# Kernel tuning notes

Measured on AMD Instinct MI355X. Metric: run time of the kernel, lower is better.

## Reference

```python
import jax, jax.numpy as jnp
import numpy as np

USER, ITEM, TAG = 100000, 50000, 20000
D = 64
LAYERS = 2
LEAKY = 0.5
KEEP = 0.9
E_ADJ, E_TAG, E_SOC = 2_000_000, 1_000_000, 1_000_000


def _xavier(k, shape):
    bound = float(np.sqrt(6.0 / (shape[0] + shape[1])))
    return jax.random.uniform(k, shape, jnp.float32, -bound, bound)


def setup_inputs() -> dict:
    key = jax.random.key(0)
    ks = jax.random.split(key, 12)
    N = USER + ITEM   # interaction graph nodes
    M = ITEM + TAG    # tag graph nodes
    return {
        "uEmbeds": _xavier(ks[0], (USER, D)),
        "iEmbeds": _xavier(ks[1], (ITEM, D)),
        "tEmbeds": _xavier(ks[2], (TAG, D)),
        "adj_rows": jax.random.randint(ks[3], (E_ADJ,), 0, N, jnp.int32),
        "adj_cols": jax.random.randint(ks[4], (E_ADJ,), 0, N, jnp.int32),
        "adj_vals": jax.random.uniform(ks[5], (E_ADJ,), jnp.float32) * 0.01,
        "tag_rows": jax.random.randint(ks[6], (E_TAG,), 0, M, jnp.int32),
        "tag_cols": jax.random.randint(ks[7], (E_TAG,), 0, M, jnp.int32),
        "tag_vals": jax.random.uniform(ks[8], (E_TAG,), jnp.float32) * 0.01,
        "soc_rows": jax.random.randint(ks[9], (E_SOC,), 0, USER, jnp.int32),
        "soc_cols": jax.random.randint(ks[10], (E_SOC,), 0, USER, jnp.int32),
        "soc_vals": jax.random.uniform(ks[11], (E_SOC,), jnp.float32) * 0.01,
    }


def _drop_edge(vals, k):
    # SpAdjDropEdge: keep each edge w.p. KEEP, rescale kept values by 1/KEEP.
    # Masking values to 0 is equivalent to removing edges from the spmm.
    mask = jnp.floor(jax.random.uniform(k, vals.shape) + KEEP)
    return vals * mask * (1.0 / KEEP)


def _gcn(rows, cols, vals, x, n):
    # spmm: out[r] = sum_e vals[e] * x[cols[e]]  (gather-scale-scatter)
    h = jax.ops.segment_sum(vals[:, None] * x[cols], rows, num_segments=n)
    return jnp.where(h >= 0, h, LEAKY * h)  # LeakyReLU


def reference(uEmbeds, iEmbeds, tEmbeds,
              adj_rows, adj_cols, adj_vals,
              tag_rows, tag_cols, tag_vals,
              soc_rows, soc_cols, soc_vals):
    dkey = jax.random.key(42)
    lat = jnp.concatenate([uEmbeds, iEmbeds], axis=0)       # [USER+ITEM, D]
    tag_lat = jnp.concatenate([iEmbeds, tEmbeds], axis=0)   # [ITEM+TAG, D]
    acc = lat
    for i in range(LAYERS):
        k1 = jax.random.fold_in(dkey, 3 * i)
        k2 = jax.random.fold_in(dkey, 3 * i + 1)
        k3 = jax.random.fold_in(dkey, 3 * i + 2)
        tem = _gcn(adj_rows, adj_cols, _drop_edge(adj_vals, k1), lat, USER + ITEM)
        tg_in = jnp.concatenate([lat[USER:], tag_lat[ITEM:]], axis=0)
        tg = _gcn(tag_rows, tag_cols, _drop_edge(tag_vals, k2), tg_in, ITEM + TAG)
        soc = _gcn(soc_rows, soc_cols, _drop_edge(soc_vals, k3), lat[:USER], USER)
        lat = jnp.concatenate([tem[:USER] + soc, tem[USER:] + tg[:ITEM]], axis=0)
        tag_lat = tg
        acc = acc + lat
    return acc  # embeds = sum(lats), shape [USER+ITEM, D]
```

## Files before the change

### kernel.cpp

```cpp
#include <hip/hip_runtime.h>
#include <stdint.h>

#define USER_N 100000
#define ITEM_N 50000
#define TAG_N  20000
#define NN (USER_N + ITEM_N)
#define MM (ITEM_N + TAG_N)
#define DD 64
#define NT_ROWS (NN + MM + USER_N)

#define BSH 10
#define BROWS (1 << BSH)
#define NBKT0 147
#define NBKT1 167
#define NBKT (NBKT0 + NBKT1)
#define SLICES 512

__host__ __device__ __forceinline__ void tf2x32(uint32_t k0, uint32_t k1,
                                                uint32_t x0, uint32_t x1,
                                                uint32_t* o0, uint32_t* o1) {
  uint32_t ks2 = k0 ^ k1 ^ 0x1BD11BDAu;
#define ROTL32(v, d) (((v) << (d)) | ((v) >> (32 - (d))))
#define TF_RND(d) { x0 += x1; x1 = ROTL32(x1, d); x1 ^= x0; }
  x0 += k0; x1 += k1;
  TF_RND(13) TF_RND(15) TF_RND(26) TF_RND(6)
  x0 += k1;  x1 += ks2 + 1u;
  TF_RND(17) TF_RND(29) TF_RND(16) TF_RND(24)
  x0 += ks2; x1 += k0 + 2u;
  TF_RND(13) TF_RND(15) TF_RND(26) TF_RND(6)
  x0 += k0;  x1 += k1 + 3u;
  TF_RND(17) TF_RND(29) TF_RND(16) TF_RND(24)
  x0 += k1;  x1 += ks2 + 4u;
  TF_RND(13) TF_RND(15) TF_RND(26) TF_RND(6)
  x0 += ks2; x1 += k0 + 5u;
  *o0 = x0; *o1 = x1;
#undef TF_RND
#undef ROTL32
}

__device__ __forceinline__ float drop_mask(uint32_t e, uint32_t k0, uint32_t k1) {
  uint32_t o0, o1;
  tf2x32(k0, k1, 0u, e, &o0, &o1);
  uint32_t bits = o0 ^ o1;
  float u = __uint_as_float((bits >> 9) | 0x3F800000u) - 1.0f;
  return floorf(u + 0.9f);
}

__device__ __forceinline__ uint32_t f2bf(float f) {
  uint32_t u = __float_as_uint(f);
  return (u + 0x7fffu + ((u >> 16) & 1u)) >> 16;
}
__device__ __forceinline__ float bflo(uint32_t u) { return __uint_as_float(u << 16); }
__device__ __forceinline__ float bfhi(uint32_t u) { return __uint_as_float(u & 0xffff0000u); }


__global__ __launch_bounds__(1024) void hist_kernel(
    const int* __restrict__ adj_r, const int* __restrict__ tag_r,
    const int* __restrict__ soc_r, int* __restrict__ chist,
    int nAdj, int nTag, int nSoc) {
  __shared__ int cnt[NBKT1];
  int tid = threadIdx.x, k = blockIdx.x;
  int r = (k >= SLICES) ? 1 : 0;
  int kk = k - r * SLICES;
  int nTot = r ? (nTag + nSoc) : nAdj;
  int nBkt = r ? NBKT1 : NBKT0;
  int bktBase = r ? NBKT0 : 0;
  for (int b = tid; b < nBkt; b += 1024) cnt[b] = 0;
  __syncthreads();
  int per = (nTot + SLICES - 1) / SLICES;
  int e0 = kk * per;
  int e1 = e0 + per; if (e1 > nTot) e1 = nTot;
  for (int e = e0 + tid; e < e1; e += 1024) {
    int j;
    if (r == 0) j = adj_r[e];
    else if (e < nTag) j = tag_r[e];
    else j = MM + soc_r[e - nTag];
    atomicAdd(&cnt[j >> BSH], 1);
  }
  __syncthreads();
  for (int b = tid; b < nBkt; b += 1024)
    chist[(bktBase + b) * SLICES + kk] = cnt[b];
}

__global__ __launch_bounds__(512) void scanA_kernel(const int* __restrict__ chist,
                                                    int* __restrict__ btot) {
  __shared__ int red[512];
  int gb = blockIdx.x, t = threadIdx.x;
  red[t] = chist[gb * SLICES + t];
  __syncthreads();
  for (int off = 256; off > 0; off >>= 1) {
    if (t < off) red[t] += red[t + off];
    __syncthreads();
  }
  if (t == 0) btot[gb] = red[0];
}

__global__ __launch_bounds__(512) void scanB_kernel(const int* __restrict__ chist,
                                                    const int* __restrict__ btot,
                                                    int* __restrict__ boff,
                                                    int* __restrict__ bbase,
                                                    int* __restrict__ rp, int totE) {
  __shared__ int red[512];
  int gb = blockIdx.x, t = threadIdx.x;
  int rstart = (gb >= NBKT0) ? NBKT0 : 0;
  int ps = 0;
  for (int b = rstart + t; b < gb; b += 512) ps += btot[b];
  red[t] = ps;
  __syncthreads();
  for (int off = 256; off > 0; off >>= 1) {
    if (t < off) red[t] += red[t + off];
    __syncthreads();
  }
  int pb = red[0];
  __syncthreads();
  int c = chist[gb * SLICES + t];
  red[t] = c;
  __syncthreads();
  for (int off = 1; off < 512; off <<= 1) {
    int v = (t >= off) ? red[t - off] : 0;
    __syncthreads();
    red[t] += v;
    __syncthreads();
  }
  boff[gb * SLICES + t] = pb + red[t] - c;
  if (t == 0) {
    bbase[gb] = pb;
    if (gb == 0) rp[NT_ROWS] = totE;
  }
}

__global__ __launch_bounds__(1024) void bin_kernel(
    const int* __restrict__ pr, const int* __restrict__ pc, const float* __restrict__ pv,
    const int* __restrict__ sr, const int* __restrict__ scc, const float* __restrict__ sv,
    const int* __restrict__ boff, int2* __restrict__ stage,
    int nPrim, int nTot, int rowOff2, int bktBase, int nBkt,
    uint32_t pa0, uint32_t pa1, uint32_t pb0, uint32_t pb1,
    uint32_t sa0, uint32_t sa1, uint32_t sb0, uint32_t sb1) {
  __shared__ int cur[NBKT1];
  int tid = threadIdx.x, k = blockIdx.x;
  for (int b = tid; b < nBkt; b += 1024) cur[b] = boff[(bktBase + b) * SLICES + k];
  __syncthreads();
  int per = (nTot + SLICES - 1) / SLICES;
  int e0 = k * per;
  int e1 = e0 + per; if (e1 > nTot) e1 = nTot;
  const float SC = (float)(1.0 / 0.9);
  for (int e = e0 + tid; e < e1; e += 1024) {
    int j, c; float v; uint32_t le, k00, k01, k10, k11;
    if (e < nPrim) {
      le = (uint32_t)e;
      j = pr[e]; c = pc[e]; v = pv[e];
      k00 = pa0; k01 = pa1; k10 = pb0; k11 = pb1;
    } else {
      le = (uint32_t)(e - nPrim);
      j = rowOff2 + sr[e - nPrim]; c = scc[e - nPrim]; v = sv[e - nPrim];
      k00 = sa0; k01 = sa1; k10 = sb0; k11 = sb1;
    }
    uint32_t w = f2bf(v * drop_mask(le, k00, k01) * SC) |
                 (f2bf(v * drop_mask(le, k10, k11) * SC) << 16);
    int lb = j >> BSH;
    int pos = atomicAdd(&cur[lb], 1);
    stage[pos] = make_int2(c | ((j & (BROWS - 1)) << 18), (int)w);
  }
}

__global__ __launch_bounds__(512) void ls_kernel(
    int* __restrict__ rp, const int* __restrict__ bbase, const int* __restrict__ btot,
    const int2* __restrict__ stage, int2* __restrict__ rec,
    int rowStart, int rowEnd, int eBase, int bktBase) {
  __shared__ int cur[BROWS];
  __shared__ int red[512];
  int tid = threadIdx.x, lb = blockIdx.x, gb = bktBase + lb;
  int sbase = bbase[gb];
  int nst = btot[gb];
  int base = eBase + sbase;
  cur[tid] = 0; cur[tid + 512] = 0;
  __syncthreads();
  for (int i = tid; i < nst; i += 512)
    atomicAdd(&cur[((uint32_t)stage[sbase + i].x) >> 18], 1);
  __syncthreads();
  int c0 = cur[2 * tid], c1 = cur[2 * tid + 1];
  int pairs = c0 + c1;
  red[tid] = pairs;
  __syncthreads();
  for (int off = 1; off < 512; off <<= 1) {
    int v = (tid >= off) ? red[tid - off] : 0;
    __syncthreads();
    red[tid] += v;
    __syncthreads();
  }
  int excl = red[tid] - pairs;
  int r = rowStart + (lb << BSH) + 2 * tid;
  int p0 = base + excl, p1 = p0 + c0;
  if (r < rowEnd) rp[r] = p0;
  if (r + 1 < rowEnd) rp[r + 1] = p1;
  __syncthreads();
  cur[2 * tid] = p0; cur[2 * tid + 1] = p1;
  __syncthreads();
  for (int i = tid; i < nst; i += 512) {
    int2 m = stage[sbase + i];
    int pos = atomicAdd(&cur[((uint32_t)m.x) >> 18], 1);
    rec[pos] = make_int2((m.x & 0x3FFFF) * DD, m.y);
  }
}

#define FMA8(c0, c1, v, q) { \
    c0.x += v * bflo(q.x); c0.y += v * bfhi(q.x); \
    c0.z += v * bflo(q.y); c0.w += v * bfhi(q.y); \
    c1.x += v * bflo(q.z); c1.y += v * bfhi(q.z); \
    c1.z += v * bflo(q.w); c1.w += v * bfhi(q.w); }

template <int VS>
__device__ __forceinline__ void gather_sub(int s0, int s1, const int2* __restrict__ rec,
                                           const ushort* __restrict__ src,
                                           int fl, float4& A0, float4& A1) {
  float4 a0 = make_float4(0.f, 0.f, 0.f, 0.f);
  float4 a1 = make_float4(0.f, 0.f, 0.f, 0.f);
  float4 b0 = make_float4(0.f, 0.f, 0.f, 0.f);
  float4 b1 = make_float4(0.f, 0.f, 0.f, 0.f);
  const ushort* sl = src + fl * 8;
  int i = s0;
  for (; i + 8 <= s1; i += 8) {
    long long r[8];
    uint4 q[8];
#pragma unroll
    for (int u = 0; u < 8; ++u)
      r[u] = __builtin_nontemporal_load((const long long*)(rec + i + u));
#pragma unroll
    for (int u = 0; u < 8; ++u)
      q[u] = *(const uint4*)(sl + (uint32_t)r[u]);
#pragma unroll
    for (int u = 0; u < 8; ++u) {
      uint32_t w = (uint32_t)((unsigned long long)r[u] >> 32);
      float v = VS ? bfhi(w) : bflo(w);
      if (u & 1) { FMA8(b0, b1, v, q[u]) } else { FMA8(a0, a1, v, q[u]) }
    }
  }
  if (i + 4 <= s1) {
    long long r[4];
    uint4 q[4];
#pragma unroll
    for (int u = 0; u < 4; ++u)
      r[u] = __builtin_nontemporal_load((const long long*)(rec + i + u));
#pragma unroll
    for (int u = 0; u < 4; ++u)
      q[u] = *(const uint4*)(sl + (uint32_t)r[u]);
#pragma unroll
    for (int u = 0; u < 4; ++u) {
      uint32_t w = (uint32_t)((unsigned long long)r[u] >> 32);
      float v = VS ? bfhi(w) : bflo(w);
      if (u & 1) { FMA8(b0, b1, v, q[u]) } else { FMA8(a0, a1, v, q[u]) }
    }
    i += 4;
  }
  for (; i < s1; ++i) {
    long long rr = __builtin_nontemporal_load((const long long*)(rec + i));
    uint4 q = *(const uint4*)(sl + (uint32_t)rr);
    uint32_t w = (uint32_t)((unsigned long long)rr >> 32);
    float v = VS ? bfhi(w) : bflo(w);
    FMA8(a0, a1, v, q)
  }
  A0 = make_float4(a0.x + b0.x, a0.y + b0.y, a0.z + b0.z, a0.w + b0.w);
  A1 = make_float4(a1.x + b1.x, a1.y + b1.y, a1.z + b1.z, a1.w + b1.w);
}

__device__ __forceinline__ float4 lk4(float4 x) {
  x.x = x.x >= 0.0f ? x.x : 0.5f * x.x;
  x.y = x.y >= 0.0f ? x.y : 0.5f * x.y;
  x.z = x.z >= 0.0f ? x.z : 0.5f * x.z;
  x.w = x.w >= 0.0f ? x.w : 0.5f * x.w;
  return x;
}

__device__ __forceinline__ uint4 pack8(float4 a, float4 b) {
  uint4 p;
  p.x = f2bf(a.x) | (f2bf(a.y) << 16);
  p.y = f2bf(a.z) | (f2bf(a.w) << 16);
  p.z = f2bf(b.x) | (f2bf(b.y) << 16);
  p.w = f2bf(b.z) | (f2bf(b.w) << 16);
  return p;
}

template <int VS, bool FINAL, bool WITHTAG>
__global__ void gather_mega_kernel(
    const int* __restrict__ arp, const int2* __restrict__ arec,
    const int* __restrict__ srp, const int2* __restrict__ srec,
    const int* __restrict__ trp, const int2* __restrict__ trec,
    const ushort* __restrict__ lat,
    ushort* __restrict__ latOut, ushort* __restrict__ tgOut,
    float* __restrict__ acc) {
  int r = (blockIdx.x * blockDim.x + threadIdx.x) >> 3;
  int fl = threadIdx.x & 7;
  if (WITHTAG && r >= NN) {
    int rr = r - NN;
    if (rr >= TAG_N) return;
    int tr = rr + ITEM_N;
    float4 a0, a1;
    gather_sub<VS>(trp[tr], trp[tr + 1], trec, lat + (size_t)USER_N * DD, fl, a0, a1);
    ((uint4*)(tgOut + (size_t)rr * DD))[fl] = pack8(lk4(a0), lk4(a1));
    return;
  }
  if (r >= NN) return;
  float4 t0, t1, b0, b1;
  gather_sub<VS>(arp[r], arp[r + 1], arec, lat, fl, t0, t1);
  if (r < USER_N) {
    gather_sub<VS>(srp[r], srp[r + 1], srec, lat, fl, b0, b1);
  } else {
    int tr = r - USER_N;
    gather_sub<VS>(trp[tr], trp[tr + 1], trec, lat + (size_t)USER_N * DD, fl, b0, b1);
  }
  t0 = lk4(t0); t1 = lk4(t1); b0 = lk4(b0); b1 = lk4(b1);
  float4 o0 = make_float4(t0.x + b0.x, t0.y + b0.y, t0.z + b0.z, t0.w + b0.w);
  float4 o1 = make_float4(t1.x + b1.x, t1.y + b1.y, t1.z + b1.z, t1.w + b1.w);
  if (FINAL) {
    uint4 l = ((const uint4*)(lat + (size_t)r * DD))[fl];
    float4* ap = (float4*)(acc + (size_t)r * DD);
    float4 v0 = ap[fl * 2], v1 = ap[fl * 2 + 1];
    v0.x += bflo(l.x) + o0.x; v0.y += bfhi(l.x) + o0.y;
    v0.z += bflo(l.y) + o0.z; v0.w += bfhi(l.y) + o0.w;
    v1.x += bflo(l.z) + o1.x; v1.y += bfhi(l.z) + o1.y;
    v1.z += bflo(l.w) + o1.z; v1.w += bfhi(l.w) + o1.w;
    ap[fl * 2] = v0; ap[fl * 2 + 1] = v1;
  } else {
    ((uint4*)(latOut + (size_t)r * DD))[fl] = pack8(o0, o1);
  }
}

__global__ void init_kernel(const float4* __restrict__ u, const float4* __restrict__ it,
                            const float4* __restrict__ tE,
                            float4* __restrict__ acc, ushort4* __restrict__ lat0bf,
                            ushort4* __restrict__ tEmbf) {
  int idx = blockIdx.x * blockDim.x + threadIdx.x;
  const int uN = USER_N * 16, nN = NN * 16;
  if (idx < nN) {
    float4 v = (idx < uN) ? u[idx] : it[idx - uN];
    acc[idx] = v;
    ushort4 h;
    h.x = (ushort)f2bf(v.x); h.y = (ushort)f2bf(v.y);
    h.z = (ushort)f2bf(v.z); h.w = (ushort)f2bf(v.w);
    lat0bf[idx] = h;
  } else if (idx < nN + TAG_N * 16) {
    int j = idx - nN;
    float4 v = tE[j];
    ushort4 h;
    h.x = (ushort)f2bf(v.x); h.y = (ushort)f2bf(v.y);
    h.z = (ushort)f2bf(v.z); h.w = (ushort)f2bf(v.w);
    tEmbf[j] = h;
  }
}

extern "C" void kernel_launch(void* const* d_in, const int* in_sizes, int n_in,
                              void* d_out, int out_size, void* d_ws, size_t ws_size,
                              hipStream_t stream) {
  const float* uE    = (const float*)d_in[0];
  const float* iE    = (const float*)d_in[1];
  const float* tEm   = (const float*)d_in[2];
  const int*   adj_r = (const int*)d_in[3];
  const int*   adj_c = (const int*)d_in[4];
  const float* adj_v = (const float*)d_in[5];
  const int*   tag_r = (const int*)d_in[6];
  const int*   tag_c = (const int*)d_in[7];
  const float* tag_v = (const float*)d_in[8];
  const int*   soc_r = (const int*)d_in[9];
  const int*   soc_c = (const int*)d_in[10];
  const float* soc_v = (const float*)d_in[11];
  const int nAdj = in_sizes[5], nTag = in_sizes[8], nSoc = in_sizes[11];
  const int totE = nAdj + nTag + nSoc;

  float* acc = (float*)d_out;

  ushort* lat0bf = (ushort*)d_ws;
  ushort* tEmbf  = lat0bf + (size_t)NN * DD;
  ushort* lat1bf = tEmbf  + (size_t)TAG_N * DD;
  ushort* tg1bf  = lat1bf + (size_t)NN * DD;
  int2* stage    = (int2*)lat1bf;
  int2* rec  = (int2*)(tg1bf + (size_t)TAG_N * DD);
  int*  ip   = (int*)(rec + totE);
  int* chist = ip;  ip += NBKT * SLICES;
  int* boff  = ip;  ip += NBKT * SLICES;
  int* btot  = ip;  ip += NBKT;
  int* bbase = ip;  ip += NBKT;
  int* rp    = ip;  ip += NT_ROWS + 1;

  uint32_t kk[6][2];
  for (uint32_t j = 0; j < 6; ++j) tf2x32(0u, 42u, 0u, j, &kk[j][0], &kk[j][1]);

  const int thr = 256;
#define CDIV(a, b) (((a) + (b) - 1) / (b))

  hist_kernel<<<2 * SLICES, 1024, 0, stream>>>(adj_r, tag_r, soc_r, chist,
                                               nAdj, nTag, nSoc);
  scanA_kernel<<<NBKT, 512, 0, stream>>>(chist, btot);
  scanB_kernel<<<NBKT, 512, 0, stream>>>(chist, btot, boff, bbase, rp, totE);
  bin_kernel<<<SLICES, 1024, 0, stream>>>(
      adj_r, adj_c, adj_v, adj_r, adj_c, adj_v,
      boff, stage, nAdj, nAdj, 0, 0, NBKT0,
      kk[0][0], kk[0][1], kk[3][0], kk[3][1], 0u, 0u, 0u, 0u);
  ls_kernel<<<NBKT0, 512, 0, stream>>>(rp, bbase, btot, stage, rec, 0, NN, 0, 0);
  bin_kernel<<<SLICES, 1024, 0, stream>>>(
      tag_r, tag_c, tag_v, soc_r, soc_c, soc_v,
      boff, stage, nTag, nTag + nSoc, MM, NBKT0, NBKT1,
      kk[1][0], kk[1][1], kk[4][0], kk[4][1],
      kk[2][0], kk[2][1], kk[5][0], kk[5][1]);
  ls_kernel<<<NBKT1, 512, 0, stream>>>(rp, bbase, btot, stage, rec, NN, NT_ROWS, nAdj, NBKT0);

  init_kernel<<<CDIV((NN + TAG_N) * 16, thr), thr, 0, stream>>>(
      (const float4*)uE, (const float4*)iE, (const float4*)tEm,
      (float4*)acc, (ushort4*)lat0bf, (ushort4*)tEmbf);

  const int* arp = rp;
  const int* trp = rp + NN;
  const int* srp = rp + NN + MM;
  gather_mega_kernel<0, false, true><<<CDIV((NN + TAG_N) * 8, thr), thr, 0, stream>>>(
      arp, rec, srp, rec, trp, rec, lat0bf, lat1bf, tg1bf, nullptr);

  gather_mega_kernel<1, true, false><<<CDIV(NN * 8, thr), thr, 0, stream>>>(
      arp, rec, srp, rec, trp, rec, lat1bf, nullptr, nullptr, acc);
#undef CDIV
}
```

Before: 419.2 us.

## Sort edges within rows by column chunk and fuse init into histogram kernel

The local-sort kernel now counts and scatters edges into (row, column-chunk) sub-buckets, so each row's edges come out ordered by coarse column range. The aim is better cache locality for the later gathers of source embeddings. Separately, the embedding init and bf16 conversion work moves into extra blocks of the histogram kernel, removing one launch. The cost is a 10x larger shared-memory counter array and more atomics and scan work in the local sort.

```diff
diff --git a/kernel.cpp b/kernel.cpp
--- a/kernel.cpp
+++ b/kernel.cpp
@@ -15,6 +15,8 @@
 #define NBKT1 167
 #define NBKT (NBKT0 + NBKT1)
 #define SLICES 512
+#define NCH 10
+#define CSH2 14
 
 __host__ __device__ __forceinline__ void tf2x32(uint32_t k0, uint32_t k1,
                                                 uint32_t x0, uint32_t x1,
@@ -54,12 +56,35 @@
 __device__ __forceinline__ float bfhi(uint32_t u) { return __uint_as_float(u & 0xffff0000u); }
 
 
-__global__ __launch_bounds__(1024) void hist_kernel(
+__global__ __launch_bounds__(1024) void histinit_kernel(
     const int* __restrict__ adj_r, const int* __restrict__ tag_r,
     const int* __restrict__ soc_r, int* __restrict__ chist,
-    int nAdj, int nTag, int nSoc) {
+    int nAdj, int nTag, int nSoc,
+    const float4* __restrict__ u, const float4* __restrict__ it,
+    const float4* __restrict__ tE, float4* __restrict__ acc,
+    ushort4* __restrict__ lat0bf, ushort4* __restrict__ tEmbf) {
   __shared__ int cnt[NBKT1];
   int tid = threadIdx.x, k = blockIdx.x;
+  if (k >= 2 * SLICES) {
+    int idx = (k - 2 * SLICES) * 1024 + tid;
+    const int uN = USER_N * 16, nN = NN * 16;
+    if (idx < nN) {
+      float4 v = (idx < uN) ? u[idx] : it[idx - uN];
+      acc[idx] = v;
+      ushort4 h;
+      h.x = (ushort)f2bf(v.x); h.y = (ushort)f2bf(v.y);
+      h.z = (ushort)f2bf(v.z); h.w = (ushort)f2bf(v.w);
+      lat0bf[idx] = h;
+    } else if (idx < nN + TAG_N * 16) {
+      int j = idx - nN;
+      float4 v = tE[j];
+      ushort4 h;
+      h.x = (ushort)f2bf(v.x); h.y = (ushort)f2bf(v.y);
+      h.z = (ushort)f2bf(v.z); h.w = (ushort)f2bf(v.w);
+      tEmbf[j] = h;
+    }
+    return;
+  }
   int r = (k >= SLICES) ? 1 : 0;
   int kk = k - r * SLICES;
   int nTot = r ? (nTag + nSoc) : nAdj;
@@ -167,20 +192,26 @@
     int* __restrict__ rp, const int* __restrict__ bbase, const int* __restrict__ btot,
     const int2* __restrict__ stage, int2* __restrict__ rec,
     int rowStart, int rowEnd, int eBase, int bktBase) {
-  __shared__ int cur[BROWS];
+  __shared__ int cur[BROWS * NCH];
   __shared__ int red[512];
   int tid = threadIdx.x, lb = blockIdx.x, gb = bktBase + lb;
   int sbase = bbase[gb];
   int nst = btot[gb];
   int base = eBase + sbase;
-  cur[tid] = 0; cur[tid + 512] = 0;
-  __syncthreads();
-  for (int i = tid; i < nst; i += 512)
-    atomicAdd(&cur[((uint32_t)stage[sbase + i].x) >> 18], 1);
-  __syncthreads();
-  int c0 = cur[2 * tid], c1 = cur[2 * tid + 1];
-  int pairs = c0 + c1;
-  red[tid] = pairs;
+  for (int i = tid; i < BROWS * NCH; i += 512) cur[i] = 0;
+  __syncthreads();
+  for (int i = tid; i < nst; i += 512) {
+    int mx = stage[sbase + i].x;
+    atomicAdd(&cur[(((uint32_t)mx) >> 18) * NCH + ((mx & 0x3FFFF) >> CSH2)], 1);
+  }
+  __syncthreads();
+  const int PT = (BROWS * NCH) / 512;
+  int loc[PT];
+  int s = 0;
+  int o0 = tid * PT;
+#pragma unroll
+  for (int u = 0; u < PT; ++u) { loc[u] = s; s += cur[o0 + u]; }
+  red[tid] = s;
   __syncthreads();
   for (int off = 1; off < 512; off <<= 1) {
     int v = (tid >= off) ? red[tid - off] : 0;
@@ -188,18 +219,23 @@
     red[tid] += v;
     __syncthreads();
   }
-  int excl = red[tid] - pairs;
-  int r = rowStart + (lb << BSH) + 2 * tid;
-  int p0 = base + excl, p1 = p0 + c0;
-  if (r < rowEnd) rp[r] = p0;
-  if (r + 1 < rowEnd) rp[r + 1] = p1;
-  __syncthreads();
-  cur[2 * tid] = p0; cur[2 * tid + 1] = p1;
+  int excl = red[tid] - s;
+#pragma unroll
+  for (int u = 0; u < PT; ++u) {
+    int idx = o0 + u;
+    int p = base + excl + loc[u];
+    cur[idx] = p;
+    if ((idx % NCH) == 0) {
+      int r = rowStart + (lb << BSH) + idx / NCH;
+      if (r < rowEnd) rp[r] = p;
+    }
+  }
   __syncthreads();
   for (int i = tid; i < nst; i += 512) {
     int2 m = stage[sbase + i];
-    int pos = atomicAdd(&cur[((uint32_t)m.x) >> 18], 1);
-    rec[pos] = make_int2((m.x & 0x3FFFF) * DD, m.y);
+    int col = m.x & 0x3FFFF;
+    int pos = atomicAdd(&cur[(((uint32_t)m.x) >> 18) * NCH + (col >> CSH2)], 1);
+    rec[pos] = make_int2(col * DD, m.y);
   }
 }
 
@@ -325,29 +361,6 @@
   }
 }
 
-__global__ void init_kernel(const float4* __restrict__ u, const float4* __restrict__ it,
-                            const float4* __restrict__ tE,
-                            float4* __restrict__ acc, ushort4* __restrict__ lat0bf,
-                            ushort4* __restrict__ tEmbf) {
-  int idx = blockIdx.x * blockDim.x + threadIdx.x;
-  const int uN = USER_N * 16, nN = NN * 16;
-  if (idx < nN) {
-    float4 v = (idx < uN) ? u[idx] : it[idx - uN];
-    acc[idx] = v;
-    ushort4 h;
-    h.x = (ushort)f2bf(v.x); h.y = (ushort)f2bf(v.y);
-    h.z = (ushort)f2bf(v.z); h.w = (ushort)f2bf(v.w);
-    lat0bf[idx] = h;
-  } else if (idx < nN + TAG_N * 16) {
-    int j = idx - nN;
-    float4 v = tE[j];
-    ushort4 h;
-    h.x = (ushort)f2bf(v.x); h.y = (ushort)f2bf(v.y);
-    h.z = (ushort)f2bf(v.z); h.w = (ushort)f2bf(v.w);
-    tEmbf[j] = h;
-  }
-}
-
 extern "C" void kernel_launch(void* const* d_in, const int* in_sizes, int n_in,
                               void* d_out, int out_size, void* d_ws, size_t ws_size,
                               hipStream_t stream) {
@@ -387,8 +400,11 @@
   const int thr = 256;
 #define CDIV(a, b) (((a) + (b) - 1) / (b))
 
-  hist_kernel<<<2 * SLICES, 1024, 0, stream>>>(adj_r, tag_r, soc_r, chist,
-                                               nAdj, nTag, nSoc);
+  int initBlocks = CDIV((NN + TAG_N) * 16, 1024);
+  histinit_kernel<<<2 * SLICES + initBlocks, 1024, 0, stream>>>(
+      adj_r, tag_r, soc_r, chist, nAdj, nTag, nSoc,
+      (const float4*)uE, (const float4*)iE, (const float4*)tEm,
+      (float4*)acc, (ushort4*)lat0bf, (ushort4*)tEmbf);
   scanA_kernel<<<NBKT, 512, 0, stream>>>(chist, btot);
   scanB_kernel<<<NBKT, 512, 0, stream>>>(chist, btot, boff, bbase, rp, totE);
   bin_kernel<<<SLICES, 1024, 0, stream>>>(
@@ -403,10 +419,6 @@
       kk[2][0], kk[2][1], kk[5][0], kk[5][1]);
   ls_kernel<<<NBKT1, 512, 0, stream>>>(rp, bbase, btot, stage, rec, NN, NT_ROWS, nAdj, NBKT0);
 
-  init_kernel<<<CDIV((NN + TAG_N) * 16, thr), thr, 0, stream>>>(
-      (const float4*)uE, (const float4*)iE, (const float4*)tEm,
-      (float4*)acc, (ushort4*)lat0bf, (ushort4*)tEmbf);
-
   const int* arp = rp;
   const int* trp = rp + NN;
   const int* srp = rp + NN + MM;
```

Result: no change. 415.5 us (-0.9%).

## Merge hist/init and both bin/ls rounds into single launches; drop acc init

Applied to the files above, without the earlier changes.

Folds the bf16 conversion of the embeddings into the histogram kernel. The two binning passes now run as one launch, using the output buffer as a second staging area, and the two local-sort passes are likewise merged into one launch. The fp32 acc initialisation is removed: the final gather reads the original user/item embeddings directly instead of re-reading acc. The gather inner loop becomes a single 16-wide unrolled masked loop with no 8/4/1 tails, which issues padded loads up to 16 past the end, hence the extra 16 elements reserved after rec. This cuts launches and serialization and removes one full fp32 write and read, at the cost of wasted gather loads on short rows.

```diff
diff --git a/kernel.cpp b/kernel.cpp
--- a/kernel.cpp
+++ b/kernel.cpp
@@ -54,12 +54,34 @@
 __device__ __forceinline__ float bfhi(uint32_t u) { return __uint_as_float(u & 0xffff0000u); }
 
 
-__global__ __launch_bounds__(1024) void hist_kernel(
+__global__ __launch_bounds__(1024) void histinit_kernel(
     const int* __restrict__ adj_r, const int* __restrict__ tag_r,
     const int* __restrict__ soc_r, int* __restrict__ chist,
-    int nAdj, int nTag, int nSoc) {
+    int nAdj, int nTag, int nSoc,
+    const float4* __restrict__ u, const float4* __restrict__ it,
+    const float4* __restrict__ tE,
+    ushort4* __restrict__ lat0bf, ushort4* __restrict__ tEmbf) {
   __shared__ int cnt[NBKT1];
   int tid = threadIdx.x, k = blockIdx.x;
+  if (k >= 2 * SLICES) {
+    int idx = (k - 2 * SLICES) * 1024 + tid;
+    const int uN = USER_N * 16, nN = NN * 16;
+    if (idx < nN) {
+      float4 v = (idx < uN) ? u[idx] : it[idx - uN];
+      ushort4 h;
+      h.x = (ushort)f2bf(v.x); h.y = (ushort)f2bf(v.y);
+      h.z = (ushort)f2bf(v.z); h.w = (ushort)f2bf(v.w);
+      lat0bf[idx] = h;
+    } else if (idx < nN + TAG_N * 16) {
+      int j = idx - nN;
+      float4 v = tE[j];
+      ushort4 h;
+      h.x = (ushort)f2bf(v.x); h.y = (ushort)f2bf(v.y);
+      h.z = (ushort)f2bf(v.z); h.w = (ushort)f2bf(v.w);
+      tEmbf[j] = h;
+    }
+    return;
+  }
   int r = (k >= SLICES) ? 1 : 0;
   int kk = k - r * SLICES;
   int nTot = r ? (nTag + nSoc) : nAdj;
@@ -129,31 +151,43 @@
   }
 }
 
-__global__ __launch_bounds__(1024) void bin_kernel(
-    const int* __restrict__ pr, const int* __restrict__ pc, const float* __restrict__ pv,
-    const int* __restrict__ sr, const int* __restrict__ scc, const float* __restrict__ sv,
-    const int* __restrict__ boff, int2* __restrict__ stage,
-    int nPrim, int nTot, int rowOff2, int bktBase, int nBkt,
-    uint32_t pa0, uint32_t pa1, uint32_t pb0, uint32_t pb1,
-    uint32_t sa0, uint32_t sa1, uint32_t sb0, uint32_t sb1) {
+__global__ __launch_bounds__(1024) void bin01_kernel(
+    const int* __restrict__ adj_r, const int* __restrict__ adj_c, const float* __restrict__ adj_v,
+    const int* __restrict__ tag_r, const int* __restrict__ tag_c, const float* __restrict__ tag_v,
+    const int* __restrict__ soc_r, const int* __restrict__ soc_c, const float* __restrict__ soc_v,
+    const int* __restrict__ boff, int2* __restrict__ stage0, int2* __restrict__ stage1,
+    int nAdj, int nTag, int nSoc,
+    uint32_t a0, uint32_t a1, uint32_t a2, uint32_t a3,
+    uint32_t t0, uint32_t t1, uint32_t t2, uint32_t t3,
+    uint32_t s0, uint32_t s1, uint32_t s2, uint32_t s3) {
   __shared__ int cur[NBKT1];
   int tid = threadIdx.x, k = blockIdx.x;
-  for (int b = tid; b < nBkt; b += 1024) cur[b] = boff[(bktBase + b) * SLICES + k];
+  int rnd = (k >= SLICES) ? 1 : 0;
+  int kk = k - rnd * SLICES;
+  int nTot = rnd ? (nTag + nSoc) : nAdj;
+  int nBkt = rnd ? NBKT1 : NBKT0;
+  int bktBase = rnd ? NBKT0 : 0;
+  int2* stage = rnd ? stage1 : stage0;
+  for (int b = tid; b < nBkt; b += 1024) cur[b] = boff[(bktBase + b) * SLICES + kk];
   __syncthreads();
   int per = (nTot + SLICES - 1) / SLICES;
-  int e0 = k * per;
+  int e0 = kk * per;
   int e1 = e0 + per; if (e1 > nTot) e1 = nTot;
   const float SC = (float)(1.0 / 0.9);
   for (int e = e0 + tid; e < e1; e += 1024) {
     int j, c; float v; uint32_t le, k00, k01, k10, k11;
-    if (e < nPrim) {
+    if (rnd == 0) {
       le = (uint32_t)e;
-      j = pr[e]; c = pc[e]; v = pv[e];
-      k00 = pa0; k01 = pa1; k10 = pb0; k11 = pb1;
+      j = adj_r[e]; c = adj_c[e]; v = adj_v[e];
+      k00 = a0; k01 = a1; k10 = a2; k11 = a3;
+    } else if (e < nTag) {
+      le = (uint32_t)e;
+      j = tag_r[e]; c = tag_c[e]; v = tag_v[e];
+      k00 = t0; k01 = t1; k10 = t2; k11 = t3;
     } else {
-      le = (uint32_t)(e - nPrim);
-      j = rowOff2 + sr[e - nPrim]; c = scc[e - nPrim]; v = sv[e - nPrim];
-      k00 = sa0; k01 = sa1; k10 = sb0; k11 = sb1;
+      le = (uint32_t)(e - nTag);
+      j = MM + soc_r[e - nTag]; c = soc_c[e - nTag]; v = soc_v[e - nTag];
+      k00 = s0; k01 = s1; k10 = s2; k11 = s3;
     }
     uint32_t w = f2bf(v * drop_mask(le, k00, k01) * SC) |
                  (f2bf(v * drop_mask(le, k10, k11) * SC) << 16);
@@ -163,13 +197,19 @@
   }
 }
 
-__global__ __launch_bounds__(512) void ls_kernel(
+__global__ __launch_bounds__(512) void ls01_kernel(
     int* __restrict__ rp, const int* __restrict__ bbase, const int* __restrict__ btot,
-    const int2* __restrict__ stage, int2* __restrict__ rec,
-    int rowStart, int rowEnd, int eBase, int bktBase) {
+    const int2* __restrict__ stage0, const int2* __restrict__ stage1,
+    int2* __restrict__ rec, int nAdj) {
   __shared__ int cur[BROWS];
   __shared__ int red[512];
-  int tid = threadIdx.x, lb = blockIdx.x, gb = bktBase + lb;
+  int tid = threadIdx.x, gb = blockIdx.x;
+  int rnd = (gb >= NBKT0) ? 1 : 0;
+  int lb = rnd ? gb - NBKT0 : gb;
+  const int2* stage = rnd ? stage1 : stage0;
+  int rowStart = rnd ? NN : 0;
+  int rowEnd = rnd ? NT_ROWS : NN;
+  int eBase = rnd ? nAdj : 0;
   int sbase = bbase[gb];
   int nst = btot[gb];
   int base = eBase + sbase;
@@ -218,46 +258,25 @@
   float4 b0 = make_float4(0.f, 0.f, 0.f, 0.f);
   float4 b1 = make_float4(0.f, 0.f, 0.f, 0.f);
   const ushort* sl = src + fl * 8;
-  int i = s0;
-  for (; i + 8 <= s1; i += 8) {
-    long long r[8];
-    uint4 q[8];
+  for (int i = s0; i < s1; i += 16) {
+    int n = s1 - i;
+    long long r[16];
 #pragma unroll
-    for (int u = 0; u < 8; ++u)
+    for (int u = 0; u < 16; ++u)
       r[u] = __builtin_nontemporal_load((const long long*)(rec + i + u));
+    uint4 q[16];
 #pragma unroll
-    for (int u = 0; u < 8; ++u)
-      q[u] = *(const uint4*)(sl + (uint32_t)r[u]);
+    for (int u = 0; u < 16; ++u) {
+      uint32_t off = (u < n) ? (uint32_t)r[u] : 0u;
+      q[u] = *(const uint4*)(sl + off);
+    }
 #pragma unroll
-    for (int u = 0; u < 8; ++u) {
+    for (int u = 0; u < 16; ++u) {
       uint32_t w = (uint32_t)((unsigned long long)r[u] >> 32);
       float v = VS ? bfhi(w) : bflo(w);
+      v = (u < n) ? v : 0.0f;
       if (u & 1) { FMA8(b0, b1, v, q[u]) } else { FMA8(a0, a1, v, q[u]) }
     }
-  }
-  if (i + 4 <= s1) {
-    long long r[4];
-    uint4 q[4];
-#pragma unroll
-    for (int u = 0; u < 4; ++u)
-      r[u] = __builtin_nontemporal_load((const long long*)(rec + i + u));
-#pragma unroll
-    for (int u = 0; u < 4; ++u)
-      q[u] = *(const uint4*)(sl + (uint32_t)r[u]);
-#pragma unroll
-    for (int u = 0; u < 4; ++u) {
-      uint32_t w = (uint32_t)((unsigned long long)r[u] >> 32);
-      float v = VS ? bfhi(w) : bflo(w);
-      if (u & 1) { FMA8(b0, b1, v, q[u]) } else { FMA8(a0, a1, v, q[u]) }
-    }
-    i += 4;
-  }
-  for (; i < s1; ++i) {
-    long long rr = __builtin_nontemporal_load((const long long*)(rec + i));
-    uint4 q = *(const uint4*)(sl + (uint32_t)rr);
-    uint32_t w = (uint32_t)((unsigned long long)rr >> 32);
-    float v = VS ? bfhi(w) : bflo(w);
-    FMA8(a0, a1, v, q)
   }
   A0 = make_float4(a0.x + b0.x, a0.y + b0.y, a0.z + b0.z, a0.w + b0.w);
   A1 = make_float4(a1.x + b1.x, a1.y + b1.y, a1.z + b1.z, a1.w + b1.w);
@@ -286,6 +305,7 @@
     const int* __restrict__ srp, const int2* __restrict__ srec,
     const int* __restrict__ trp, const int2* __restrict__ trec,
     const ushort* __restrict__ lat,
+    const float* __restrict__ uE, const float* __restrict__ iE,
     ushort* __restrict__ latOut, ushort* __restrict__ tgOut,
     float* __restrict__ acc) {
   int r = (blockIdx.x * blockDim.x + threadIdx.x) >> 3;
@@ -313,38 +333,18 @@
   float4 o1 = make_float4(t1.x + b1.x, t1.y + b1.y, t1.z + b1.z, t1.w + b1.w);
   if (FINAL) {
     uint4 l = ((const uint4*)(lat + (size_t)r * DD))[fl];
-    float4* ap = (float4*)(acc + (size_t)r * DD);
-    float4 v0 = ap[fl * 2], v1 = ap[fl * 2 + 1];
+    const float4* e0 = (r < USER_N)
+        ? (const float4*)(uE + (size_t)r * DD)
+        : (const float4*)(iE + (size_t)(r - USER_N) * DD);
+    float4 v0 = e0[fl * 2], v1 = e0[fl * 2 + 1];
     v0.x += bflo(l.x) + o0.x; v0.y += bfhi(l.x) + o0.y;
     v0.z += bflo(l.y) + o0.z; v0.w += bfhi(l.y) + o0.w;
     v1.x += bflo(l.z) + o1.x; v1.y += bfhi(l.z) + o1.y;
     v1.z += bflo(l.w) + o1.z; v1.w += bfhi(l.w) + o1.w;
+    float4* ap = (float4*)(acc + (size_t)r * DD);
     ap[fl * 2] = v0; ap[fl * 2 + 1] = v1;
   } else {
     ((uint4*)(latOut + (size_t)r * DD))[fl] = pack8(o0, o1);
-  }
-}
-
-__global__ void init_kernel(const float4* __restrict__ u, const float4* __restrict__ it,
-                            const float4* __restrict__ tE,
-                            float4* __restrict__ acc, ushort4* __restrict__ lat0bf,
-                            ushort4* __restrict__ tEmbf) {
-  int idx = blockIdx.x * blockDim.x + threadIdx.x;
-  const int uN = USER_N * 16, nN = NN * 16;
-  if (idx < nN) {
-    float4 v = (idx < uN) ? u[idx] : it[idx - uN];
-    acc[idx] = v;
-    ushort4 h;
-    h.x = (ushort)f2bf(v.x); h.y = (ushort)f2bf(v.y);
-    h.z = (ushort)f2bf(v.z); h.w = (ushort)f2bf(v.w);
-    lat0bf[idx] = h;
-  } else if (idx < nN + TAG_N * 16) {
-    int j = idx - nN;
-    float4 v = tE[j];
-    ushort4 h;
-    h.x = (ushort)f2bf(v.x); h.y = (ushort)f2bf(v.y);
-    h.z = (ushort)f2bf(v.z); h.w = (ushort)f2bf(v.w);
-    tEmbf[j] = h;
   }
 }
 
@@ -372,9 +372,10 @@
   ushort* tEmbf  = lat0bf + (size_t)NN * DD;
   ushort* lat1bf = tEmbf  + (size_t)TAG_N * DD;
   ushort* tg1bf  = lat1bf + (size_t)NN * DD;
-  int2* stage    = (int2*)lat1bf;
+  int2* stage0   = (int2*)lat1bf;
+  int2* stage1   = (int2*)d_out;
   int2* rec  = (int2*)(tg1bf + (size_t)TAG_N * DD);
-  int*  ip   = (int*)(rec + totE);
+  int*  ip   = (int*)(rec + totE + 16);
   int* chist = ip;  ip += NBKT * SLICES;
   int* boff  = ip;  ip += NBKT * SLICES;
   int* btot  = ip;  ip += NBKT;
@@ -387,33 +388,28 @@
   const int thr = 256;
 #define CDIV(a, b) (((a) + (b) - 1) / (b))
 
-  hist_kernel<<<2 * SLICES, 1024, 0, stream>>>(adj_r, tag_r, soc_r, chist,
-                                               nAdj, nTag, nSoc);
+  int initBlocks = CDIV((NN + TAG_N) * 16, 1024);
+  histinit_kernel<<<2 * SLICES + initBlocks, 1024, 0, stream>>>(
+      adj_r, tag_r, soc_r, chist, nAdj, nTag, nSoc,
+      (const float4*)uE, (const float4*)iE, (const float4*)tEm,
+      (ushort4*)lat0bf, (ushort4*)tEmbf);
   scanA_kernel<<<NBKT, 512, 0, stream>>>(chist, btot);
   scanB_kernel<<<NBKT, 512, 0, stream>>>(chist, btot, boff, bbase, rp, totE);
-  bin_kernel<<<SLICES, 1024, 0, stream>>>(
-      adj_r, adj_c, adj_v, adj_r, adj_c, adj_v,
-      boff, stage, nAdj, nAdj, 0, 0, NBKT0,
-      kk[0][0], kk[0][1], kk[3][0], kk[3][1], 0u, 0u, 0u, 0u);
-  ls_kernel<<<NBKT0, 512, 0, stream>>>(rp, bbase, btot, stage, rec, 0, NN, 0, 0);
-  bin_kernel<<<SLICES, 1024, 0, stream>>>(
-      tag_r, tag_c, tag_v, soc_r, soc_c, soc_v,
-      boff, stage, nTag, nTag + nSoc, MM, NBKT0, NBKT1,
+  bin01_kernel<<<2 * SLICES, 1024, 0, stream>>>(
+      adj_r, adj_c, adj_v, tag_r, tag_c, tag_v, soc_r, soc_c, soc_v,
+      boff, stage0, stage1, nAdj, nTag, nSoc,
+      kk[0][0], kk[0][1], kk[3][0], kk[3][1],
       kk[1][0], kk[1][1], kk[4][0], kk[4][1],
       kk[2][0], kk[2][1], kk[5][0], kk[5][1]);
-  ls_kernel<<<NBKT1, 512, 0, stream>>>(rp, bbase, btot, stage, rec, NN, NT_ROWS, nAdj, NBKT0);
-
-  init_kernel<<<CDIV((NN + TAG_N) * 16, thr), thr, 0, stream>>>(
-      (const float4*)uE, (const float4*)iE, (const float4*)tEm,
-      (float4*)acc, (ushort4*)lat0bf, (ushort4*)tEmbf);
+  ls01_kernel<<<NBKT, 512, 0, stream>>>(rp, bbase, btot, stage0, stage1, rec, nAdj);
 
   const int* arp = rp;
   const int* trp = rp + NN;
   const int* srp = rp + NN + MM;
   gather_mega_kernel<0, false, true><<<CDIV((NN + TAG_N) * 8, thr), thr, 0, stream>>>(
-      arp, rec, srp, rec, trp, rec, lat0bf, lat1bf, tg1bf, nullptr);
+      arp, rec, srp, rec, trp, rec, lat0bf, uE, iE, lat1bf, tg1bf, nullptr);
 
   gather_mega_kernel<1, true, false><<<CDIV(NN * 8, thr), thr, 0, stream>>>(
-      arp, rec, srp, rec, trp, rec, lat1bf, nullptr, nullptr, acc);
+      arp, rec, srp, rec, trp, rec, lat1bf, uE, iE, nullptr, nullptr, acc);
 #undef CDIV
 }
```

Measured after the change: 383.5 us. 8.5% less time.
